# Kernel tuning notes

Measured on AMD Instinct MI355X. Metric: run time of the kernel, lower is better.

## Reference

```python
import jax, jax.numpy as jnp
import numpy as np

E, H, F, LE, LD, K, CD, DIN = 256, 8, 1024, 4, 3, 8, 4, 4
B, S = 16, 512
SIG2 = 1.0 ** 2 + 1e-8   # dr_sigma**2 + 1e-8
EPS = 1e-5               # LayerNorm / BatchNorm eps


def _ln(x, w, b):
    m = x.mean(-1, keepdims=True)
    v = ((x - m) ** 2).mean(-1, keepdims=True)
    return (x - m) / jnp.sqrt(v + EPS) * w + b


def _gelu(x):
    return jax.nn.gelu(x, approximate=False)  # torch nn.GELU default = exact erf


def _mha(xq, xkv, qkv_w, qkv_b, out_w, out_b, bias=None):
    # torch nn.MultiheadAttention (batch_first), additive float attn bias broadcast over heads
    wq, wk, wv = jnp.split(qkv_w, 3, axis=0)
    bq, bk, bv = jnp.split(qkv_b, 3)
    q = xq @ wq.T + bq
    k = xkv @ wk.T + bk
    v = xkv @ wv.T + bv
    Bn, Tq, Tk = q.shape[0], q.shape[1], k.shape[1]
    hd = E // H
    qh = q.reshape(Bn, Tq, H, hd)
    kh = k.reshape(Bn, Tk, H, hd)
    vh = v.reshape(Bn, Tk, H, hd)
    s = jnp.einsum('bqhd,bkhd->bhqk', qh, kh) / jnp.sqrt(jnp.asarray(hd, q.dtype))
    if bias is not None:
        s = s + bias[:, None]  # same bias for every head
    p = jax.nn.softmax(s, axis=-1)
    o = jnp.einsum('bhqk,bkhd->bqhd', p, vh).reshape(Bn, Tq, E)
    return o @ out_w.T + out_b


def _forward(x, mask, parent_idx, in_w, in_b, bn_w, bn_b, dr_gamma,
             e_qkv_w, e_qkv_b, e_out_w, e_out_b, e_l1_w, e_l1_b, e_l2_w, e_l2_b,
             e_n1_w, e_n1_b, e_n2_w, e_n2_b,
             parent_w, parent_b, query_embed, c1_w, c1_b, c2_w, c2_b,
             d_sqkv_w, d_sqkv_b, d_sout_w, d_sout_b,
             d_cqkv_w, d_cqkv_b, d_cout_w, d_cout_b,
             d_l1_w, d_l1_b, d_l2_w, d_l2_b,
             d_n1_w, d_n1_b, d_n2_w, d_n2_b, d_n3_w, d_n3_b,
             child_w, child_b, o1_w, o1_b, o2_w, o2_b):
    x = jnp.nan_to_num(x)
    # input_dim==4 convention: (log_pt, dEta, dPhi, log_E)
    coords = jnp.stack([x[..., 1], x[..., 2]], axis=-1)          # [B,S,2]
    # input_proj: Linear -> BatchNorm1d (eval: mean 0, var 1) -> GELU (dropout=identity in eval)
    h = x @ in_w.T + in_b
    h = (h / jnp.sqrt(1.0 + EPS)) * bn_w + bn_b
    h = _gelu(h)
    # dR Gaussian attention bias: [B,S,S]; mask is all-valid so no -inf fill
    d = coords[:, :, None, :] - coords[:, None, :, :]
    dr2 = d[..., 0] ** 2 + d[..., 1] ** 2
    bias = -(dr_gamma[0] * dr2) / (2.0 * SIG2)
    # dR-biased pre-norm encoder
    for i in range(LE):
        hn = _ln(h, e_n1_w[i], e_n1_b[i])
        h = h + _mha(hn, hn, e_qkv_w[i], e_qkv_b[i], e_out_w[i], e_out_b[i], bias)
        hn = _ln(h, e_n2_w[i], e_n2_b[i])
        h = h + _gelu(hn @ e_l1_w[i].T + e_l1_b[i]) @ e_l2_w[i].T + e_l2_b[i]
    memory = jnp.nan_to_num(h)
    parent_logit = (memory @ parent_w.T + parent_b)[..., 0]       # [B,S]
    # conditional decoder queries
    p = memory[jnp.arange(memory.shape[0]), parent_idx]           # [B,E]
    m = mask.astype(memory.dtype)
    g = (memory * m[..., None]).sum(1) / jnp.maximum(m.sum(1, keepdims=True), 1.0)
    cond = _gelu(jnp.concatenate([p, g], -1) @ c1_w.T + c1_b) @ c2_w.T + c2_b
    t = query_embed[None] + cond[:, None]                         # [B,K,E]
    # pre-norm transformer decoder (self-attn, cross-attn, ff)
    for i in range(LD):
        tn = _ln(t, d_n1_w[i], d_n1_b[i])
        t = t + _mha(tn, tn, d_sqkv_w[i], d_sqkv_b[i], d_sout_w[i], d_sout_b[i])
        tn = _ln(t, d_n2_w[i], d_n2_b[i])
        t = t + _mha(tn, memory, d_cqkv_w[i], d_cqkv_b[i], d_cout_w[i], d_cout_b[i])
        tn = _ln(t, d_n3_w[i], d_n3_b[i])
        t = t + _gelu(tn @ d_l1_w[i].T + d_l1_b[i]) @ d_l2_w[i].T + d_l2_b[i]
    child_feat = t @ child_w.T + child_b                          # [B,K,CD]
    obj_logit = (_gelu(t @ o1_w.T + o1_b) @ o2_w.T + o2_b)[..., 0]  # [B,K]
    return parent_logit, child_feat, obj_logit


def setup_inputs() -> dict:
    key = jax.random.key(0)
    ks = iter(jax.random.split(key, 64))
    def w(shape, scale=0.05):
        return jax.random.normal(next(ks), shape, jnp.float32) * scale
    return {
        'x': jax.random.normal(next(ks), (B, S, DIN), jnp.float32),
        'mask': jnp.ones((B, S), dtype=bool),
        'parent_idx': jax.random.randint(next(ks), (B,), 0, S),
        'in_w': w((E, DIN)), 'in_b': jnp.zeros((E,)),
        'bn_w': jnp.ones((E,)), 'bn_b': jnp.zeros((E,)),
        'dr_gamma': jnp.ones((1,)),
        'e_qkv_w': w((LE, 3 * E, E)), 'e_qkv_b': jnp.zeros((LE, 3 * E)),
        'e_out_w': w((LE, E, E)), 'e_out_b': jnp.zeros((LE, E)),
        'e_l1_w': w((LE, F, E)), 'e_l1_b': jnp.zeros((LE, F)),
        'e_l2_w': w((LE, E, F)), 'e_l2_b': jnp.zeros((LE, E)),
        'e_n1_w': jnp.ones((LE, E)), 'e_n1_b': jnp.zeros((LE, E)),
        'e_n2_w': jnp.ones((LE, E)), 'e_n2_b': jnp.zeros((LE, E)),
        'parent_w': w((1, E)), 'parent_b': jnp.zeros((1,)),
        'query_embed': w((K, E), 0.02),
        'c1_w': w((E, 2 * E)), 'c1_b': jnp.zeros((E,)),
        'c2_w': w((E, E)), 'c2_b': jnp.zeros((E,)),
        'd_sqkv_w': w((LD, 3 * E, E)), 'd_sqkv_b': jnp.zeros((LD, 3 * E)),
        'd_sout_w': w((LD, E, E)), 'd_sout_b': jnp.zeros((LD, E)),
        'd_cqkv_w': w((LD, 3 * E, E)), 'd_cqkv_b': jnp.zeros((LD, 3 * E)),
        'd_cout_w': w((LD, E, E)), 'd_cout_b': jnp.zeros((LD, E)),
        'd_l1_w': w((LD, F, E)), 'd_l1_b': jnp.zeros((LD, F)),
        'd_l2_w': w((LD, E, F)), 'd_l2_b': jnp.zeros((LD, E)),
        'd_n1_w': jnp.ones((LD, E)), 'd_n1_b': jnp.zeros((LD, E)),
        'd_n2_w': jnp.ones((LD, E)), 'd_n2_b': jnp.zeros((LD, E)),
        'd_n3_w': jnp.ones((LD, E)), 'd_n3_b': jnp.zeros((LD, E)),
        'child_w': w((CD, E)), 'child_b': jnp.zeros((CD,)),
        'o1_w': w((E, E)), 'o1_b': jnp.zeros((E,)),
        'o2_w': w((1, E)), 'o2_b': jnp.zeros((1,)),
    }


def reference(x, mask, parent_idx, in_w, in_b, bn_w, bn_b, dr_gamma,
              e_qkv_w, e_qkv_b, e_out_w, e_out_b, e_l1_w, e_l1_b, e_l2_w, e_l2_b,
              e_n1_w, e_n1_b, e_n2_w, e_n2_b,
              parent_w, parent_b, query_embed, c1_w, c1_b, c2_w, c2_b,
              d_sqkv_w, d_sqkv_b, d_sout_w, d_sout_b,
              d_cqkv_w, d_cqkv_b, d_cout_w, d_cout_b,
              d_l1_w, d_l1_b, d_l2_w, d_l2_b,
              d_n1_w, d_n1_b, d_n2_w, d_n2_b, d_n3_w, d_n3_b,
              child_w, child_b, o1_w, o1_b, o2_w, o2_b):
    return _forward(x, mask, parent_idx, in_w, in_b, bn_w, bn_b, dr_gamma,
                    e_qkv_w, e_qkv_b, e_out_w, e_out_b, e_l1_w, e_l1_b, e_l2_w, e_l2_b,
                    e_n1_w, e_n1_b, e_n2_w, e_n2_b,
                    parent_w, parent_b, query_embed, c1_w, c1_b, c2_w, c2_b,
                    d_sqkv_w, d_sqkv_b, d_sout_w, d_sout_b,
                    d_cqkv_w, d_cqkv_b, d_cout_w, d_cout_b,
                    d_l1_w, d_l1_b, d_l2_w, d_l2_b,
                    d_n1_w, d_n1_b, d_n2_w, d_n2_b, d_n3_w, d_n3_b,
                    child_w, child_b, o1_w, o1_b, o2_w, o2_b)
```

## Files before the change

kernel.cpp:

```cpp
#include <hip/hip_runtime.h>
#include <math.h>

#define E 256
#define H 8
#define HD 32
#define FF 1024
#define LE 4
#define LDN 3
#define KQ 8
#define CDIM 4
#define DIN 4
#define BATCH 16
#define SEQ 512

typedef __attribute__((ext_vector_type(8))) short s8b;
typedef __attribute__((ext_vector_type(4))) float f32x4;

__device__ __forceinline__ float gelu_f(float x) {
  return 0.5f * x * (1.f + erff(x * 0.70710678118654752f));
}

__device__ __forceinline__ unsigned short f2b(float f) {
  union { float f; unsigned u; } a;
  a.f = f;
  unsigned r = (a.u + 0x7fffu + ((a.u >> 16) & 1u)) >> 16;
  return (unsigned short)r;
}

__device__ __forceinline__ float b2f(unsigned short u) {
  union { unsigned u; float f; } a;
  a.u = ((unsigned)u) << 16;
  return a.f;
}

__device__ __forceinline__ void gload16(const unsigned short* g, unsigned short* l) {
  __builtin_amdgcn_global_load_lds((const __attribute__((address_space(1))) void*)g,
                                   (__attribute__((address_space(3))) void*)l, 16, 0, 0);
}

template <int GELU, int RESID, int OMODE>
__global__ __launch_bounds__(256) void mfma_gemm_kernel(
    const unsigned short* __restrict__ A, const unsigned short* __restrict__ Wt,
    const float* __restrict__ bias, const float* __restrict__ resid,
    float* __restrict__ outf, unsigned short* __restrict__ outb,
    unsigned short* __restrict__ vtb,
    int M, int N, int K) {
  __shared__ __align__(16) unsigned short As[128 * 32];
  __shared__ __align__(16) unsigned short Bs[128 * 32];
  int tid = threadIdx.x;
  int lane = tid & 63, w = tid >> 6;
  int row0 = blockIdx.y * 128, col0 = blockIdx.x * 128;
  int wr = (w >> 1) * 64, wc = (w & 1) * 64;
  f32x4 acc[4][4] = {};

  int sr0 = w * 32 + (lane >> 2);
  int sr1 = sr0 + 16;
  int sc = lane & 3;
  int gc0 = (sc ^ ((sr0 >> 1) & 3)) * 8;
  int gc1 = (sc ^ ((sr1 >> 1) & 3)) * 8;
  const unsigned short* Ap0 = A + (size_t)(row0 + sr0) * K + gc0;
  const unsigned short* Ap1 = A + (size_t)(row0 + sr1) * K + gc1;
  const unsigned short* Bp0 = Wt + (size_t)(col0 + sr0) * K + gc0;
  const unsigned short* Bp1 = Wt + (size_t)(col0 + sr1) * K + gc1;
  unsigned short* lA0 = As + (w * 32) * 32;
  unsigned short* lA1 = As + (w * 32 + 16) * 32;
  unsigned short* lB0 = Bs + (w * 32) * 32;
  unsigned short* lB1 = Bs + (w * 32 + 16) * 32;

  for (int k0 = 0; k0 < K; k0 += 32) {
    __syncthreads();
    gload16(Ap0 + k0, lA0);
    gload16(Ap1 + k0, lA1);
    gload16(Bp0 + k0, lB0);
    gload16(Bp1 + k0, lB1);
    __syncthreads();
    int krow = lane & 15, kq = lane >> 4;
    s8b afr[4], bfr[4];
    #pragma unroll
    for (int mi = 0; mi < 4; ++mi) {
      int r = wr + mi * 16 + krow;
      afr[mi] = *(const s8b*)(As + r * 32 + ((kq ^ ((r >> 1) & 3)) * 8));
    }
    #pragma unroll
    for (int ni = 0; ni < 4; ++ni) {
      int r = wc + ni * 16 + krow;
      bfr[ni] = *(const s8b*)(Bs + r * 32 + ((kq ^ ((r >> 1) & 3)) * 8));
    }
    #pragma unroll
    for (int mi = 0; mi < 4; ++mi)
      #pragma unroll
      for (int ni = 0; ni < 4; ++ni)
        acc[mi][ni] = __builtin_amdgcn_mfma_f32_16x16x32_bf16(afr[mi], bfr[ni], acc[mi][ni], 0, 0, 0);
  }

  int cl = lane & 15, rb = (lane >> 4) * 4;
  #pragma unroll
  for (int ni = 0; ni < 4; ++ni) {
    int col = col0 + wc + ni * 16 + cl;
    float bv = bias[col];
    #pragma unroll
    for (int mi = 0; mi < 4; ++mi) {
      #pragma unroll
      for (int j = 0; j < 4; ++j) {
        int row = row0 + wr + mi * 16 + rb + j;
        float v = acc[mi][ni][j] + bv;
        if (RESID) v += resid[(size_t)row * N + col];
        if (GELU) v = gelu_f(v);
        if (OMODE == 0) {
          outf[(size_t)row * N + col] = v;
        } else if (OMODE == 1) {
          outb[(size_t)row * N + col] = f2b(v);
        } else {
          int b = row >> 9, s = row & 511;
          int sect = col >> 8, hh = (col >> 5) & 7, d = col & 31;
          if (sect < 2)
            outb[((((size_t)sect * BATCH + b) * H + hh) * SEQ + s) * HD + d] = f2b(v);
          else
            vtb[(((size_t)b * H + hh) * HD + d) * SEQ + s] = f2b(v);
        }
      }
    }
  }
}

__global__ __launch_bounds__(256) void mfma_gemm64_kernel(
    const unsigned short* __restrict__ A, const unsigned short* __restrict__ Wt,
    const float* __restrict__ bias, const float* __restrict__ resid,
    float* __restrict__ outf, int M, int N, int K) {
  __shared__ __align__(16) unsigned short As[64 * 32];
  __shared__ __align__(16) unsigned short Bs[128 * 32];
  int tid = threadIdx.x;
  int lane = tid & 63, w = tid >> 6;
  int row0 = blockIdx.y * 64, col0 = blockIdx.x * 128;
  int wr = (w >> 1) * 32, wc = (w & 1) * 64;
  f32x4 acc[2][4] = {};

  int sc = lane & 3;
  int srA = w * 16 + (lane >> 2);
  int gcA = (sc ^ ((srA >> 1) & 3)) * 8;
  const unsigned short* ApA = A + (size_t)(row0 + srA) * K + gcA;
  unsigned short* lA = As + (w * 16) * 32;
  int sr0 = w * 32 + (lane >> 2);
  int sr1 = sr0 + 16;
  int gc0 = (sc ^ ((sr0 >> 1) & 3)) * 8;
  int gc1 = (sc ^ ((sr1 >> 1) & 3)) * 8;
  const unsigned short* Bp0 = Wt + (size_t)(col0 + sr0) * K + gc0;
  const unsigned short* Bp1 = Wt + (size_t)(col0 + sr1) * K + gc1;
  unsigned short* lB0 = Bs + (w * 32) * 32;
  unsigned short* lB1 = Bs + (w * 32 + 16) * 32;

  for (int k0 = 0; k0 < K; k0 += 32) {
    __syncthreads();
    gload16(ApA + k0, lA);
    gload16(Bp0 + k0, lB0);
    gload16(Bp1 + k0, lB1);
    __syncthreads();
    int krow = lane & 15, kq = lane >> 4;
    s8b afr[2], bfr[4];
    #pragma unroll
    for (int mi = 0; mi < 2; ++mi) {
      int r = wr + mi * 16 + krow;
      afr[mi] = *(const s8b*)(As + r * 32 + ((kq ^ ((r >> 1) & 3)) * 8));
    }
    #pragma unroll
    for (int ni = 0; ni < 4; ++ni) {
      int r = wc + ni * 16 + krow;
      bfr[ni] = *(const s8b*)(Bs + r * 32 + ((kq ^ ((r >> 1) & 3)) * 8));
    }
    #pragma unroll
    for (int mi = 0; mi < 2; ++mi)
      #pragma unroll
      for (int ni = 0; ni < 4; ++ni)
        acc[mi][ni] = __builtin_amdgcn_mfma_f32_16x16x32_bf16(afr[mi], bfr[ni], acc[mi][ni], 0, 0, 0);
  }

  int cl = lane & 15, rb = (lane >> 4) * 4;
  #pragma unroll
  for (int ni = 0; ni < 4; ++ni) {
    int col = col0 + wc + ni * 16 + cl;
    float bv = bias[col];
    #pragma unroll
    for (int mi = 0; mi < 2; ++mi) {
      #pragma unroll
      for (int j = 0; j < 4; ++j) {
        int row = row0 + wr + mi * 16 + rb + j;
        float v = acc[mi][ni][j] + bv + resid[(size_t)row * N + col];
        outf[(size_t)row * N + col] = v;
      }
    }
  }
}

__global__ __launch_bounds__(256) void mfma_attn_kernel(
    const unsigned short* __restrict__ qkb, const unsigned short* __restrict__ vt,
    const float2* __restrict__ carr, const float* __restrict__ gamma_p,
    unsigned short* __restrict__ out) {
  __shared__ __align__(16) unsigned short P[4][16 * 64];
  int tid = threadIdx.x, lane = tid & 63, w = tid >> 6;
  int qt = blockIdx.x, h = blockIdx.y, b = blockIdx.z;
  int q0 = qt * 64 + w * 16;
  const unsigned short* qh = qkb + (((size_t)b * H + h) * SEQ) * HD;
  const unsigned short* kh = qkb + ((((size_t)BATCH + b) * H + h) * SEQ) * HD;
  const unsigned short* vh = vt + (((size_t)b * H + h) * HD) * SEQ;
  int r16 = lane & 15, q4 = lane >> 4;
  s8b qa = *(const s8b*)(qh + (size_t)(q0 + r16) * HD + q4 * 8);
  float eq[4], pq[4];
  #pragma unroll
  for (int j = 0; j < 4; ++j) {
    float2 c = carr[b * SEQ + q0 + q4 * 4 + j];
    eq[j] = c.x; pq[j] = c.y;
  }
  float gam = gamma_p[0] * 0.49999999500000004f;
  const float scale = 0.17677669529663687f;
  float m[4], lsum[4];
  #pragma unroll
  for (int j = 0; j < 4; ++j) { m[j] = -1e30f; lsum[j] = 0.f; }
  f32x4 o0 = {}, o1 = {};
  const f32x4 zf = {0.f, 0.f, 0.f, 0.f};
  unsigned short* pw = &P[w][0];

  for (int t = 0; t < SEQ / 64; ++t) {
    int k0 = t * 64;
    f32x4 sf[4];
    #pragma unroll
    for (int f = 0; f < 4; ++f) {
      s8b bk = *(const s8b*)(kh + (size_t)(k0 + f * 16 + r16) * HD + q4 * 8);
      sf[f] = __builtin_amdgcn_mfma_f32_16x16x32_bf16(qa, bk, zf, 0, 0, 0);
    }
    float ek[4], pk[4];
    #pragma unroll
    for (int f = 0; f < 4; ++f) {
      float2 c = carr[b * SEQ + k0 + f * 16 + r16];
      ek[f] = c.x; pk[f] = c.y;
    }
    float sc_[4][4];
    float tmax[4] = {-1e30f, -1e30f, -1e30f, -1e30f};
    #pragma unroll
    for (int f = 0; f < 4; ++f)
      #pragma unroll
      for (int j = 0; j < 4; ++j) {
        float de = eq[j] - ek[f], dp = pq[j] - pk[f];
        float v = sf[f][j] * scale - gam * (de * de + dp * dp);
        sc_[f][j] = v;
        tmax[j] = fmaxf(tmax[j], v);
      }
    #pragma unroll
    for (int j = 0; j < 4; ++j) {
      #pragma unroll
      for (int off = 1; off < 16; off <<= 1)
        tmax[j] = fmaxf(tmax[j], __shfl_xor(tmax[j], off));
      float mn = fmaxf(m[j], tmax[j]);
      float al = __expf(m[j] - mn);
      m[j] = mn;
      lsum[j] *= al;
      o0[j] *= al;
      o1[j] *= al;
    }
    __syncthreads();
    #pragma unroll
    for (int f = 0; f < 4; ++f)
      #pragma unroll
      for (int j = 0; j < 4; ++j) {
        float p = __expf(sc_[f][j] - m[j]);
        lsum[j] += p;
        int prow = q4 * 4 + j;
        int c = f * 16 + r16;
        int chunk = (c >> 3) ^ (prow & 7);
        pw[prow * 64 + chunk * 8 + (c & 7)] = f2b(p);
      }
    __syncthreads();
    #pragma unroll
    for (int ks = 0; ks < 2; ++ks) {
      int chunk = (ks * 4 + q4) ^ (r16 & 7);
      s8b pa = *(const s8b*)(pw + r16 * 64 + chunk * 8);
      s8b v0 = *(const s8b*)(vh + (size_t)r16 * SEQ + k0 + ks * 32 + q4 * 8);
      s8b v1 = *(const s8b*)(vh + (size_t)(16 + r16) * SEQ + k0 + ks * 32 + q4 * 8);
      o0 = __builtin_amdgcn_mfma_f32_16x16x32_bf16(pa, v0, o0, 0, 0, 0);
      o1 = __builtin_amdgcn_mfma_f32_16x16x32_bf16(pa, v1, o1, 0, 0, 0);
    }
  }
  #pragma unroll
  for (int j = 0; j < 4; ++j) {
    #pragma unroll
    for (int off = 1; off < 16; off <<= 1)
      lsum[j] += __shfl_xor(lsum[j], off);
    float inv = 1.f / lsum[j];
    size_t rbase = ((size_t)(b * SEQ + q0 + q4 * 4 + j)) * E + h * HD;
    out[rbase + r16] = f2b(o0[j] * inv);
    out[rbase + 16 + r16] = f2b(o1[j] * inv);
  }
}

__global__ void coords_kernel(const float* __restrict__ x, float2* __restrict__ carr) {
  int i = blockIdx.x * 256 + threadIdx.x;
  if (i >= BATCH * SEQ) return;
  carr[i] = make_float2(x[(size_t)i * DIN + 1], x[(size_t)i * DIN + 2]);
}

__global__ void f2b_kernel(const float* __restrict__ in, unsigned short* __restrict__ out, int n4) {
  int i = blockIdx.x * 256 + threadIdx.x;
  if (i >= n4) return;
  float4 v = ((const float4*)in)[i];
  ushort4 o;
  o.x = f2b(v.x); o.y = f2b(v.y); o.z = f2b(v.z); o.w = f2b(v.w);
  ((ushort4*)out)[i] = o;
}

__global__ void kvw_remap_kernel(const float* __restrict__ w, const float* __restrict__ b,
                                 unsigned short* __restrict__ wout, float* __restrict__ bout) {
  int i = blockIdx.x * 256 + threadIdx.x;
  if (i < 1536) bout[i] = b[(i >> 9) * 768 + 256 + (i & 511)];
  if (i >= 98304) return;
  int row = i >> 6, cc = i & 63;
  int l = row >> 9, rr = row & 511;
  const float* src = w + ((size_t)l * 768 + 256 + rr) * 256 + cc * 4;
  float4 v = *(const float4*)src;
  ushort4 o;
  o.x = f2b(v.x); o.y = f2b(v.y); o.z = f2b(v.z); o.w = f2b(v.w);
  *(ushort4*)(wout + (size_t)row * 256 + cc * 4) = o;
}


template <int N, int GELU>
__global__ __launch_bounds__(256) void dec_ln_gemv_kernel(
    const float* __restrict__ t, const float* __restrict__ nw, const float* __restrict__ nb,
    const float* __restrict__ W, const float* __restrict__ bias, float* __restrict__ outg) {
  __shared__ float X[8][256];
  __shared__ float Pp[4][64][9];
  int b = blockIdx.x, by = blockIdx.y, tid = threadIdx.x;
  const float* tg = t + (size_t)b * 2048;
  int w = tid >> 6, l = tid & 63;
  #pragma unroll
  for (int rr = 0; rr < 2; ++rr) {
    int r = w * 2 + rr;
    float v0 = tg[r * 256 + l], v1 = tg[r * 256 + 64 + l];
    float v2 = tg[r * 256 + 128 + l], v3 = tg[r * 256 + 192 + l];
    float s = v0 + v1 + v2 + v3;
    for (int o = 32; o > 0; o >>= 1) s += __shfl_xor(s, o);
    float mean = s * (1.f / 256);
    float d0 = v0 - mean, d1 = v1 - mean, d2 = v2 - mean, d3 = v3 - mean;
    float var = d0 * d0 + d1 * d1 + d2 * d2 + d3 * d3;
    for (int o = 32; o > 0; o >>= 1) var += __shfl_xor(var, o);
    float inv = rsqrtf(var * (1.f / 256) + 1e-5f);
    X[r][l] = d0 * inv * nw[l] + nb[l];
    X[r][l + 64] = d1 * inv * nw[l + 64] + nb[l + 64];
    X[r][l + 128] = d2 * inv * nw[l + 128] + nb[l + 128];
    X[r][l + 192] = d3 * inv * nw[l + 192] + nb[l + 192];
  }
  __syncthreads();
  int j = tid & 63, kq = tid >> 6;
  int col = by * 64 + j;
  const float4* wp = (const float4*)(W + (size_t)col * 256 + kq * 64);
  float acc[8] = {};
  #pragma unroll
  for (int kk = 0; kk < 16; ++kk) {
    float4 wv = wp[kk];
    int base = kq * 64 + kk * 4;
    #pragma unroll
    for (int r = 0; r < 8; ++r) {
      float4 xv = *(const float4*)&X[r][base];
      acc[r] += xv.x * wv.x + xv.y * wv.y + xv.z * wv.z + xv.w * wv.w;
    }
  }
  #pragma unroll
  for (int r = 0; r < 8; ++r) Pp[kq][j][r] = acc[r];
  __syncthreads();
  for (int i = tid; i < 512; i += 256) {
    int r = i & 7, j2 = i >> 3;
    float v = Pp[0][j2][r] + Pp[1][j2][r] + Pp[2][j2][r] + Pp[3][j2][r] + bias[by * 64 + j2];
    if (GELU) v = gelu_f(v);
    outg[((size_t)b * 8 + r) * N + by * 64 + j2] = v;
  }
}

__global__ __launch_bounds__(256) void dec_selfattn_sout_kernel(
    const float* __restrict__ qkvg, const float* __restrict__ W, const float* __restrict__ bias,
    float* __restrict__ t) {
  __shared__ float QK[8][768];
  __shared__ float S[512];
  __shared__ float X[8][256];
  __shared__ float Pp[4][64][9];
  int b = blockIdx.x, by = blockIdx.y, tid = threadIdx.x;
  const float* qg = qkvg + (size_t)b * 8 * 768;
  for (int i = tid; i < 6144; i += 256) ((float*)QK)[i] = qg[i];
  __syncthreads();
  for (int t2 = tid; t2 < 512; t2 += 256) {
    int h = t2 >> 6, q = (t2 >> 3) & 7, k = t2 & 7;
    const float* qp = &QK[q][h * 32];
    const float* kp = &QK[k][256 + h * 32];
    float d = 0.f;
    #pragma unroll
    for (int jj = 0; jj < 32; ++jj) d += qp[jj] * kp[jj];
    S[t2] = d * 0.17677669529663687f;
  }
  __syncthreads();
  if (tid < 64) {
    float* row = &S[tid * 8];
    float m = row[0];
    #pragma unroll
    for (int k = 1; k < 8; ++k) m = fmaxf(m, row[k]);
    float sum = 0.f;
    #pragma unroll
    for (int k = 0; k < 8; ++k) { float e = __expf(row[k] - m); row[k] = e; sum += e; }
    float inv = 1.f / sum;
    #pragma unroll
    for (int k = 0; k < 8; ++k) row[k] *= inv;
  }
  __syncthreads();
  for (int i = tid; i < 2048; i += 256) {
    int q = i >> 8, c = i & 255, h = c >> 5;
    const float* pr = &S[h * 64 + q * 8];
    float acc = 0.f;
    #pragma unroll
    for (int k = 0; k < 8; ++k) acc += pr[k] * QK[k][512 + c];
    X[q][c] = acc;
  }
  __syncthreads();
  int j = tid & 63, kq = tid >> 6;
  int col = by * 64 + j;
  const float4* wp = (const float4*)(W + (size_t)col * 256 + kq * 64);
  float acc[8] = {};
  #pragma unroll
  for (int kk = 0; kk < 16; ++kk) {
    float4 wv = wp[kk];
    int base = kq * 64 + kk * 4;
    #pragma unroll
    for (int r = 0; r < 8; ++r) {
      float4 xv = *(const float4*)&X[r][base];
      acc[r] += xv.x * wv.x + xv.y * wv.y + xv.z * wv.z + xv.w * wv.w;
    }
  }
  #pragma unroll
  for (int r = 0; r < 8; ++r) Pp[kq][j][r] = acc[r];
  __syncthreads();
  for (int i = tid; i < 512; i += 256) {
    int r = i & 7, j2 = i >> 3;
    float v = Pp[0][j2][r] + Pp[1][j2][r] + Pp[2][j2][r] + Pp[3][j2][r] + bias[by * 64 + j2];
    t[((size_t)b * 8 + r) * 256 + by * 64 + j2] += v;
  }
}

__global__ __launch_bounds__(256) void dec_gemv_resid_kernel(
    const float* __restrict__ Xg, const float* __restrict__ W, const float* __restrict__ bias,
    float* __restrict__ t) {
  __shared__ float X[8][256];
  __shared__ float Pp[4][64][9];
  int b = blockIdx.x, by = blockIdx.y, tid = threadIdx.x;
  const float* xg = Xg + (size_t)b * 2048;
  for (int i = tid; i < 2048; i += 256) ((float*)X)[i] = xg[i];
  __syncthreads();
  int j = tid & 63, kq = tid >> 6;
  int col = by * 64 + j;
  const float4* wp = (const float4*)(W + (size_t)col * 256 + kq * 64);
  float acc[8] = {};
  #pragma unroll
  for (int kk = 0; kk < 16; ++kk) {
    float4 wv = wp[kk];
    int base = kq * 64 + kk * 4;
    #pragma unroll
    for (int r = 0; r < 8; ++r) {
      float4 xv = *(const float4*)&X[r][base];
      acc[r] += xv.x * wv.x + xv.y * wv.y + xv.z * wv.z + xv.w * wv.w;
    }
  }
  #pragma unroll
  for (int r = 0; r < 8; ++r) Pp[kq][j][r] = acc[r];
  __syncthreads();
  for (int i = tid; i < 512; i += 256) {
    int r = i & 7, j2 = i >> 3;
    float v = Pp[0][j2][r] + Pp[1][j2][r] + Pp[2][j2][r] + Pp[3][j2][r] + bias[by * 64 + j2];
    t[((size_t)b * 8 + r) * 256 + by * 64 + j2] += v;
  }
}

__global__ __launch_bounds__(256) void dec_ffn2_kernel(
    const float* __restrict__ MIDg, const float* __restrict__ W, const float* __restrict__ bias,
    float* __restrict__ t) {
  __shared__ float X[8][1024];
  __shared__ float Pp[4][64][9];
  int b = blockIdx.x, by = blockIdx.y, tid = threadIdx.x;
  const float* xg = MIDg + (size_t)b * 8192;
  for (int i = tid; i < 8192; i += 256) ((float*)X)[i] = xg[i];
  __syncthreads();
  int j = tid & 63, kq = tid >> 6;
  int col = by * 64 + j;
  const float4* wp = (const float4*)(W + (size_t)col * 1024 + kq * 256);
  float acc[8] = {};
  #pragma unroll 8
  for (int kk = 0; kk < 64; ++kk) {
    float4 wv = wp[kk];
    int base = kq * 256 + kk * 4;
    #pragma unroll
    for (int r = 0; r < 8; ++r) {
      float4 xv = *(const float4*)&X[r][base];
      acc[r] += xv.x * wv.x + xv.y * wv.y + xv.z * wv.z + xv.w * wv.w;
    }
  }
  #pragma unroll
  for (int r = 0; r < 8; ++r) Pp[kq][j][r] = acc[r];
  __syncthreads();
  for (int i = tid; i < 512; i += 256) {
    int r = i & 7, j2 = i >> 3;
    float v = Pp[0][j2][r] + Pp[1][j2][r] + Pp[2][j2][r] + Pp[3][j2][r] + bias[by * 64 + j2];
    t[((size_t)b * 8 + r) * 256 + by * 64 + j2] += v;
  }
}

__global__ __launch_bounds__(256) void cross_attn_kernel(
    const float* __restrict__ Q, const unsigned short* __restrict__ KV,
    int koff, int voff, float* __restrict__ out) {
  __shared__ float sv[512];
  __shared__ float red[256];
  __shared__ float qv[32];
  __shared__ float pvred[8][32];
  int tid = threadIdx.x;
  int bid = blockIdx.x;
  int q = bid % KQ;
  int h = (bid / KQ) % H;
  int b = bid / (KQ * H);
  if (tid < 32) qv[tid] = Q[((size_t)(b * KQ + q)) * E + h * HD + tid];
  __syncthreads();
  const float scale = 0.17677669529663687f;
  for (int k = tid; k < SEQ; k += 256) {
    const unsigned short* kp = KV + ((size_t)(b * SEQ + k)) * 1536 + koff + h * HD;
    float d = 0.f;
    #pragma unroll
    for (int j4 = 0; j4 < 4; ++j4) {
      s8b kv8 = *(const s8b*)(kp + j4 * 8);
      #pragma unroll
      for (int j = 0; j < 8; ++j)
        d += qv[j4 * 8 + j] * b2f((unsigned short)kv8[j]);
    }
    sv[k] = d * scale;
  }
  __syncthreads();
  float m = -1e30f;
  for (int k = tid; k < SEQ; k += 256) m = fmaxf(m, sv[k]);
  red[tid] = m; __syncthreads();
  for (int s = 128; s > 0; s >>= 1) {
    if (tid < s) red[tid] = fmaxf(red[tid], red[tid + s]);
    __syncthreads();
  }
  m = red[0]; __syncthreads();
  float lsum = 0.f;
  for (int k = tid; k < SEQ; k += 256) { float e = __expf(sv[k] - m); sv[k] = e; lsum += e; }
  red[tid] = lsum; __syncthreads();
  for (int s = 128; s > 0; s >>= 1) {
    if (tid < s) red[tid] += red[tid + s];
    __syncthreads();
  }
  float denom = red[0];
  int d = tid & 31, g = tid >> 5;
  float acc = 0.f;
  for (int k = g; k < SEQ; k += 8)
    acc += sv[k] * b2f(KV[((size_t)(b * SEQ + k)) * 1536 + voff + h * HD + d]);
  pvred[g][d] = acc;
  __syncthreads();
  if (tid < 32) {
    float r = 0.f;
    #pragma unroll
    for (int gg = 0; gg < 8; ++gg) r += pvred[gg][tid];
    out[((size_t)(b * KQ + q)) * E + h * HD + tid] = r / denom;
  }
}

__global__ void ln_bf16_kernel(const float* __restrict__ in, const float* __restrict__ w,
                               const float* __restrict__ b, unsigned short* __restrict__ out) {
  int r = blockIdx.x;
  int l = threadIdx.x;
  const float* p = in + (size_t)r * E;
  float v0 = p[l], v1 = p[l + 64], v2 = p[l + 128], v3 = p[l + 192];
  float s = v0 + v1 + v2 + v3;
  for (int off = 32; off > 0; off >>= 1) s += __shfl_xor(s, off);
  float mean = s * (1.f / E);
  float d0 = v0 - mean, d1 = v1 - mean, d2 = v2 - mean, d3 = v3 - mean;
  float var = d0 * d0 + d1 * d1 + d2 * d2 + d3 * d3;
  for (int off = 32; off > 0; off >>= 1) var += __shfl_xor(var, off);
  float inv = rsqrtf(var * (1.f / E) + 1e-5f);
  unsigned short* o = out + (size_t)r * E;
  o[l]       = f2b(d0 * inv * w[l]       + b[l]);
  o[l + 64]  = f2b(d1 * inv * w[l + 64]  + b[l + 64]);
  o[l + 128] = f2b(d2 * inv * w[l + 128] + b[l + 128]);
  o[l + 192] = f2b(d3 * inv * w[l + 192] + b[l + 192]);
}

__global__ void input_proj_kernel(const float* __restrict__ x, const float* __restrict__ in_w,
                                  const float* __restrict__ in_b, const float* __restrict__ bn_w,
                                  const float* __restrict__ bn_b, float* __restrict__ h) {
  int idx = blockIdx.x * 256 + threadIdx.x;
  int row = idx >> 8, e = idx & 255;
  const float* xr = x + (size_t)row * DIN;
  float v = in_b[e];
  #pragma unroll
  for (int i = 0; i < DIN; ++i) v += xr[i] * in_w[e * DIN + i];
  v = v * (1.0f / sqrtf(1.0f + 1e-5f)) * bn_w[e] + bn_b[e];
  h[idx] = gelu_f(v);
}

__global__ __launch_bounds__(256) void pool_gather_kernel(
    const float* __restrict__ mem, const int* __restrict__ pidx, float* __restrict__ pg) {
  __shared__ float red[8][32];
  int b = blockIdx.x, cy = blockIdx.y, tid = threadIdx.x;
  int c = cy * 32 + (tid & 31), g = tid >> 5;
  float s = 0.f;
  for (int r = g; r < SEQ; r += 8)
    s += mem[((size_t)b * SEQ + r) * E + c];
  red[g][tid & 31] = s;
  __syncthreads();
  if (tid < 32) {
    float t = 0.f;
    #pragma unroll
    for (int g2 = 0; g2 < 8; ++g2) t += red[g2][tid];
    pg[(size_t)b * 512 + 256 + cy * 32 + tid] = t * (1.f / SEQ);
    pg[(size_t)b * 512 + cy * 32 + tid] = mem[((size_t)b * SEQ + pidx[b]) * E + cy * 32 + tid];
  }
}

__global__ void cond_kernel(const float* __restrict__ pg, const float* __restrict__ c1w,
                            const float* __restrict__ c1b, const float* __restrict__ c2w,
                            const float* __restrict__ c2b, const float* __restrict__ qe,
                            float* __restrict__ t) {
  __shared__ float PG[512];
  __shared__ float C1[256];
  int b = blockIdx.x, c = threadIdx.x;
  PG[c] = pg[(size_t)b * 512 + c];
  PG[c + 256] = pg[(size_t)b * 512 + 256 + c];
  __syncthreads();
  const float4* wp = (const float4*)(c1w + (size_t)c * 512);
  float acc = c1b[c];
  #pragma unroll 8
  for (int kk = 0; kk < 128; ++kk) {
    float4 wv = wp[kk];
    int base = kk * 4;
    acc += PG[base] * wv.x + PG[base + 1] * wv.y + PG[base + 2] * wv.z + PG[base + 3] * wv.w;
  }
  C1[c] = gelu_f(acc);
  __syncthreads();
  const float4* wp2 = (const float4*)(c2w + (size_t)c * 256);
  float acc2 = c2b[c];
  #pragma unroll 8
  for (int kk = 0; kk < 64; ++kk) {
    float4 wv = wp2[kk];
    int base = kk * 4;
    acc2 += C1[base] * wv.x + C1[base + 1] * wv.y + C1[base + 2] * wv.z + C1[base + 3] * wv.w;
  }
  #pragma unroll
  for (int k = 0; k < KQ; ++k)
    t[((size_t)b * KQ + k) * E + c] = qe[k * E + c] + acc2;
}

__global__ void head_kernel(const float* __restrict__ t,
                            const float* __restrict__ childw, const float* __restrict__ childb,
                            const float* __restrict__ o1w, const float* __restrict__ o1b,
                            const float* __restrict__ o2w, const float* __restrict__ o2b,
                            float* __restrict__ out_child, float* __restrict__ out_obj) {
  __shared__ float tr[256];
  __shared__ float red[256];
  int r = blockIdx.x, c = threadIdx.x;
  tr[c] = t[(size_t)r * E + c];
  __syncthreads();
  const float4* wp = (const float4*)(o1w + (size_t)c * 256);
  float acc = o1b[c];
  #pragma unroll 8
  for (int kk = 0; kk < 64; ++kk) {
    float4 wv = wp[kk];
    int base = kk * 4;
    acc += tr[base] * wv.x + tr[base + 1] * wv.y + tr[base + 2] * wv.z + tr[base + 3] * wv.w;
  }
  red[c] = gelu_f(acc) * o2w[c];
  __syncthreads();
  for (int s = 128; s > 0; s >>= 1) {
    if (c < s) red[c] += red[c + s];
    __syncthreads();
  }
  if (c == 0) out_obj[r] = red[0] + o2b[0];
  __syncthreads();
  #pragma unroll
  for (int j = 0; j < CDIM; ++j) {
    red[c] = tr[c] * childw[j * E + c];
    __syncthreads();
    for (int s = 128; s > 0; s >>= 1) {
      if (c < s) red[c] += red[c + s];
      __syncthreads();
    }
    if (c == 0) out_child[r * CDIM + j] = red[0] + childb[j];
    __syncthreads();
  }
}

__global__ void rowdot_kernel(const float* __restrict__ A, const float* __restrict__ w,
                              const float* __restrict__ bias, float* __restrict__ out) {
  int r = blockIdx.x, l = threadIdx.x;
  const float* p = A + (size_t)r * E;
  float s = p[l] * w[l] + p[l + 64] * w[l + 64] + p[l + 128] * w[l + 128] + p[l + 192] * w[l + 192];
  for (int off = 32; off > 0; off >>= 1) s += __shfl_xor(s, off);
  if (l == 0) out[r] = s + bias[0];
}

extern "C" void kernel_launch(void* const* d_in, const int* in_sizes, int n_in,
                              void* d_out, int out_size, void* d_ws, size_t ws_size,
                              hipStream_t stream) {
  const float* x          = (const float*)d_in[0];
  const int*   parent_idx = (const int*)d_in[2];
  const float* in_w  = (const float*)d_in[3];
  const float* in_b  = (const float*)d_in[4];
  const float* bn_w  = (const float*)d_in[5];
  const float* bn_b  = (const float*)d_in[6];
  const float* dr_gamma = (const float*)d_in[7];
  const float* e_qkv_w = (const float*)d_in[8];
  const float* e_qkv_b = (const float*)d_in[9];
  const float* e_out_w = (const float*)d_in[10];
  const float* e_out_b = (const float*)d_in[11];
  const float* e_l1_w = (const float*)d_in[12];
  const float* e_l1_b = (const float*)d_in[13];
  const float* e_l2_w = (const float*)d_in[14];
  const float* e_l2_b = (const float*)d_in[15];
  const float* e_n1_w = (const float*)d_in[16];
  const float* e_n1_b = (const float*)d_in[17];
  const float* e_n2_w = (const float*)d_in[18];
  const float* e_n2_b = (const float*)d_in[19];
  const float* parent_w = (const float*)d_in[20];
  const float* parent_b = (const float*)d_in[21];
  const float* query_embed = (const float*)d_in[22];
  const float* c1_w = (const float*)d_in[23];
  const float* c1_b = (const float*)d_in[24];
  const float* c2_w = (const float*)d_in[25];
  const float* c2_b = (const float*)d_in[26];
  const float* d_sqkv_w = (const float*)d_in[27];
  const float* d_sqkv_b = (const float*)d_in[28];
  const float* d_sout_w = (const float*)d_in[29];
  const float* d_sout_b = (const float*)d_in[30];
  const float* d_cqkv_w = (const float*)d_in[31];
  const float* d_cqkv_b = (const float*)d_in[32];
  const float* d_cout_w = (const float*)d_in[33];
  const float* d_cout_b = (const float*)d_in[34];
  const float* d_l1_w = (const float*)d_in[35];
  const float* d_l1_b = (const float*)d_in[36];
  const float* d_l2_w = (const float*)d_in[37];
  const float* d_l2_b = (const float*)d_in[38];
  const float* d_n1_w = (const float*)d_in[39];
  const float* d_n1_b = (const float*)d_in[40];
  const float* d_n2_w = (const float*)d_in[41];
  const float* d_n2_b = (const float*)d_in[42];
  const float* d_n3_w = (const float*)d_in[43];
  const float* d_n3_b = (const float*)d_in[44];
  const float* child_w = (const float*)d_in[45];
  const float* child_b = (const float*)d_in[46];
  const float* o1_w = (const float*)d_in[47];
  const float* o1_b = (const float*)d_in[48];
  const float* o2_w = (const float*)d_in[49];
  const float* o2_b = (const float*)d_in[50];

  float* out = (float*)d_out;
  const int ROWS = BATCH * SEQ;
  const int TROWS = BATCH * KQ;

  float* ws = (float*)d_ws;
  float* h         = ws;
  float* attnout_d = h + (size_t)ROWS * E;
  float* pg        = attnout_d + (size_t)TROWS * E;
  float* tbuf      = pg + BATCH * 2 * E;
  float* q_t       = tbuf + (size_t)TROWS * E;
  float* qkv_t     = q_t + (size_t)TROWS * E;
  float* dmid      = qkv_t + (size_t)TROWS * 3 * E;
  float* kvb3      = dmid + (size_t)TROWS * FF;
  unsigned short* kv_bf   = (unsigned short*)(kvb3 + 1536);
  unsigned short* hn_bf   = kv_bf + (size_t)ROWS * 1536;
  unsigned short* attn_bf = hn_bf + (size_t)ROWS * E;
  unsigned short* mid_bf  = attn_bf + (size_t)ROWS * E;
  unsigned short* eqkv_bf = mid_bf + (size_t)ROWS * FF;
  unsigned short* eout_bf = eqkv_bf + (size_t)LE * 3 * E * E;
  unsigned short* el1_bf  = eout_bf + (size_t)LE * E * E;
  unsigned short* el2_bf  = el1_bf + (size_t)LE * FF * E;
  unsigned short* kvw_bf  = el2_bf + (size_t)LE * E * FF;
  float2* carr = (float2*)(kvw_bf + (size_t)1536 * 256);
  unsigned short* qkb = mid_bf;
  unsigned short* vtb = mid_bf + (size_t)2 * ROWS * E;

  auto cvt = [&](const float* src, unsigned short* dst, size_t n) {
    int n4 = (int)(n / 4);
    f2b_kernel<<<(n4 + 255) / 256, 256, 0, stream>>>(src, dst, n4);
  };

  cvt(e_qkv_w, eqkv_bf, (size_t)LE * 3 * E * E);
  cvt(e_out_w, eout_bf, (size_t)LE * E * E);
  cvt(e_l1_w, el1_bf, (size_t)LE * FF * E);
  cvt(e_l2_w, el2_bf, (size_t)LE * E * FF);
  kvw_remap_kernel<<<384, 256, 0, stream>>>(d_cqkv_w, d_cqkv_b, kvw_bf, kvb3);
  coords_kernel<<<(BATCH * SEQ + 255) / 256, 256, 0, stream>>>(x, carr);

  input_proj_kernel<<<ROWS, 256, 0, stream>>>(x, in_w, in_b, bn_w, bn_b, h);

  for (int i = 0; i < LE; ++i) {
    const float* qb = e_qkv_b + (size_t)i * 3 * E;
    const float* ob = e_out_b + (size_t)i * E;
    const float* l1b = e_l1_b + (size_t)i * FF;
    const float* l2b = e_l2_b + (size_t)i * E;
    ln_bf16_kernel<<<ROWS, 64, 0, stream>>>(h, e_n1_w + i * E, e_n1_b + i * E, hn_bf);
    mfma_gemm_kernel<0, 0, 2><<<dim3(6, 64), 256, 0, stream>>>(
        hn_bf, eqkv_bf + (size_t)i * 3 * E * E, qb, nullptr, nullptr, qkb, vtb, ROWS, 3 * E, E);
    mfma_attn_kernel<<<dim3(SEQ / 64, H, BATCH), 256, 0, stream>>>(qkb, vtb, carr, dr_gamma, attn_bf);
    mfma_gemm64_kernel<<<dim3(2, 128), 256, 0, stream>>>(
        attn_bf, eout_bf + (size_t)i * E * E, ob, h, h, ROWS, E, E);
    ln_bf16_kernel<<<ROWS, 64, 0, stream>>>(h, e_n2_w + i * E, e_n2_b + i * E, hn_bf);
    mfma_gemm_kernel<1, 0, 1><<<dim3(8, 64), 256, 0, stream>>>(
        hn_bf, el1_bf + (size_t)i * FF * E, l1b, nullptr, nullptr, mid_bf, nullptr, ROWS, FF, E);
    mfma_gemm64_kernel<<<dim3(2, 128), 256, 0, stream>>>(
        mid_bf, el2_bf + (size_t)i * E * FF, l2b, h, h, ROWS, E, FF);
  }

  rowdot_kernel<<<ROWS, 64, 0, stream>>>(h, parent_w, parent_b, out);

  pool_gather_kernel<<<dim3(BATCH, 8), 256, 0, stream>>>(h, parent_idx, pg);
  cond_kernel<<<BATCH, 256, 0, stream>>>(pg, c1_w, c1_b, c2_w, c2_b, query_embed, tbuf);

  cvt(h, hn_bf, (size_t)ROWS * E);
  mfma_gemm_kernel<0, 0, 1><<<dim3(12, 64), 256, 0, stream>>>(
      hn_bf, kvw_bf, kvb3, nullptr, nullptr, kv_bf, nullptr, ROWS, 3 * E * 2, E);

  for (int i = 0; i < LDN; ++i) {
    dec_ln_gemv_kernel<768, 0><<<dim3(BATCH, 12), 256, 0, stream>>>(
        tbuf, d_n1_w + i * E, d_n1_b + i * E,
        d_sqkv_w + (size_t)i * 3 * E * E, d_sqkv_b + (size_t)i * 3 * E, qkv_t);
    dec_selfattn_sout_kernel<<<dim3(BATCH, 4), 256, 0, stream>>>(
        qkv_t, d_sout_w + (size_t)i * E * E, d_sout_b + (size_t)i * E, tbuf);
    dec_ln_gemv_kernel<256, 0><<<dim3(BATCH, 4), 256, 0, stream>>>(
        tbuf, d_n2_w + i * E, d_n2_b + i * E,
        d_cqkv_w + (size_t)i * 3 * E * E, d_cqkv_b + (size_t)i * 3 * E, q_t);
    cross_attn_kernel<<<BATCH * H * KQ, 256, 0, stream>>>(
        q_t, kv_bf, i * 512, i * 512 + 256, attnout_d);
    dec_gemv_resid_kernel<<<dim3(BATCH, 4), 256, 0, stream>>>(
        attnout_d, d_cout_w + (size_t)i * E * E, d_cout_b + (size_t)i * E, tbuf);
    dec_ln_gemv_kernel<1024, 1><<<dim3(BATCH, 16), 256, 0, stream>>>(
        tbuf, d_n3_w + i * E, d_n3_b + i * E,
        d_l1_w + (size_t)i * FF * E, d_l1_b + (size_t)i * FF, dmid);
    dec_ffn2_kernel<<<dim3(BATCH, 4), 256, 0, stream>>>(
        dmid, d_l2_w + (size_t)i * E * FF, d_l2_b + (size_t)i * E, tbuf);
  }

  head_kernel<<<TROWS, 256, 0, stream>>>(tbuf, child_w, child_b, o1_w, o1_b, o2_w, o2_b,
                                         out + ROWS, out + ROWS + TROWS * CDIM);
}
```

Before: 804.9 us.

## Fuse LayerNorm into residual GEMM epilogues and retile encoder GEMMs to 64-row blocks

Residual-add GEMMs now compute full 256-wide rows per block, so the epilogue can apply the next LayerNorm and write the bf16 normalized activations directly. This removes the standalone LayerNorm kernels and the final fp32-to-bf16 conversion. The input projection also applies the first LayerNorm. The remaining GEMMs switch from 128x128 to 64x128 tiles, which doubles the grid. The trade-off is that the N=256 fused GEMM launches only 128 blocks with 16 accumulators per wave, which lowers parallelism for those GEMMs.

```diff
diff --git a/kernel.cpp b/kernel.cpp
--- a/kernel.cpp
+++ b/kernel.cpp
@@ -38,95 +38,11 @@
                                    (__attribute__((address_space(3))) void*)l, 16, 0, 0);
 }
 
-template <int GELU, int RESID, int OMODE>
-__global__ __launch_bounds__(256) void mfma_gemm_kernel(
+template <int GELU, int OMODE>
+__global__ __launch_bounds__(256) void mfma_gemm64o_kernel(
     const unsigned short* __restrict__ A, const unsigned short* __restrict__ Wt,
-    const float* __restrict__ bias, const float* __restrict__ resid,
-    float* __restrict__ outf, unsigned short* __restrict__ outb,
-    unsigned short* __restrict__ vtb,
-    int M, int N, int K) {
-  __shared__ __align__(16) unsigned short As[128 * 32];
-  __shared__ __align__(16) unsigned short Bs[128 * 32];
-  int tid = threadIdx.x;
-  int lane = tid & 63, w = tid >> 6;
-  int row0 = blockIdx.y * 128, col0 = blockIdx.x * 128;
-  int wr = (w >> 1) * 64, wc = (w & 1) * 64;
-  f32x4 acc[4][4] = {};
-
-  int sr0 = w * 32 + (lane >> 2);
-  int sr1 = sr0 + 16;
-  int sc = lane & 3;
-  int gc0 = (sc ^ ((sr0 >> 1) & 3)) * 8;
-  int gc1 = (sc ^ ((sr1 >> 1) & 3)) * 8;
-  const unsigned short* Ap0 = A + (size_t)(row0 + sr0) * K + gc0;
-  const unsigned short* Ap1 = A + (size_t)(row0 + sr1) * K + gc1;
-  const unsigned short* Bp0 = Wt + (size_t)(col0 + sr0) * K + gc0;
-  const unsigned short* Bp1 = Wt + (size_t)(col0 + sr1) * K + gc1;
-  unsigned short* lA0 = As + (w * 32) * 32;
-  unsigned short* lA1 = As + (w * 32 + 16) * 32;
-  unsigned short* lB0 = Bs + (w * 32) * 32;
-  unsigned short* lB1 = Bs + (w * 32 + 16) * 32;
-
-  for (int k0 = 0; k0 < K; k0 += 32) {
-    __syncthreads();
-    gload16(Ap0 + k0, lA0);
-    gload16(Ap1 + k0, lA1);
-    gload16(Bp0 + k0, lB0);
-    gload16(Bp1 + k0, lB1);
-    __syncthreads();
-    int krow = lane & 15, kq = lane >> 4;
-    s8b afr[4], bfr[4];
-    #pragma unroll
-    for (int mi = 0; mi < 4; ++mi) {
-      int r = wr + mi * 16 + krow;
-      afr[mi] = *(const s8b*)(As + r * 32 + ((kq ^ ((r >> 1) & 3)) * 8));
-    }
-    #pragma unroll
-    for (int ni = 0; ni < 4; ++ni) {
-      int r = wc + ni * 16 + krow;
-      bfr[ni] = *(const s8b*)(Bs + r * 32 + ((kq ^ ((r >> 1) & 3)) * 8));
-    }
-    #pragma unroll
-    for (int mi = 0; mi < 4; ++mi)
-      #pragma unroll
-      for (int ni = 0; ni < 4; ++ni)
-        acc[mi][ni] = __builtin_amdgcn_mfma_f32_16x16x32_bf16(afr[mi], bfr[ni], acc[mi][ni], 0, 0, 0);
-  }
-
-  int cl = lane & 15, rb = (lane >> 4) * 4;
-  #pragma unroll
-  for (int ni = 0; ni < 4; ++ni) {
-    int col = col0 + wc + ni * 16 + cl;
-    float bv = bias[col];
-    #pragma unroll
-    for (int mi = 0; mi < 4; ++mi) {
-      #pragma unroll
-      for (int j = 0; j < 4; ++j) {
-        int row = row0 + wr + mi * 16 + rb + j;
-        float v = acc[mi][ni][j] + bv;
-        if (RESID) v += resid[(size_t)row * N + col];
-        if (GELU) v = gelu_f(v);
-        if (OMODE == 0) {
-          outf[(size_t)row * N + col] = v;
-        } else if (OMODE == 1) {
-          outb[(size_t)row * N + col] = f2b(v);
-        } else {
-          int b = row >> 9, s = row & 511;
-          int sect = col >> 8, hh = (col >> 5) & 7, d = col & 31;
-          if (sect < 2)
-            outb[((((size_t)sect * BATCH + b) * H + hh) * SEQ + s) * HD + d] = f2b(v);
-          else
-            vtb[(((size_t)b * H + hh) * HD + d) * SEQ + s] = f2b(v);
-        }
-      }
-    }
-  }
-}
-
-__global__ __launch_bounds__(256) void mfma_gemm64_kernel(
-    const unsigned short* __restrict__ A, const unsigned short* __restrict__ Wt,
-    const float* __restrict__ bias, const float* __restrict__ resid,
-    float* __restrict__ outf, int M, int N, int K) {
+    const float* __restrict__ bias, unsigned short* __restrict__ outb,
+    unsigned short* __restrict__ vtb, int N, int K) {
   __shared__ __align__(16) unsigned short As[64 * 32];
   __shared__ __align__(16) unsigned short Bs[128 * 32];
   int tid = threadIdx.x;
@@ -184,8 +100,112 @@
       #pragma unroll
       for (int j = 0; j < 4; ++j) {
         int row = row0 + wr + mi * 16 + rb + j;
-        float v = acc[mi][ni][j] + bv + resid[(size_t)row * N + col];
-        outf[(size_t)row * N + col] = v;
+        float v = acc[mi][ni][j] + bv;
+        if (GELU) v = gelu_f(v);
+        if (OMODE == 1) {
+          outb[(size_t)row * N + col] = f2b(v);
+        } else {
+          int b = row >> 9, s = row & 511;
+          int sect = col >> 8, hh = (col >> 5) & 7, d = col & 31;
+          if (sect < 2)
+            outb[((((size_t)sect * BATCH + b) * H + hh) * SEQ + s) * HD + d] = f2b(v);
+          else
+            vtb[(((size_t)b * H + hh) * HD + d) * SEQ + s] = f2b(v);
+        }
+      }
+    }
+  }
+}
+
+template <int LNMODE>
+__global__ __launch_bounds__(256) void mfma_gemm_n256_ln_kernel(
+    const unsigned short* __restrict__ A, const unsigned short* __restrict__ Wt,
+    const float* __restrict__ bias, float* __restrict__ h,
+    const float* __restrict__ nw, const float* __restrict__ nb,
+    unsigned short* __restrict__ hn, int K) {
+  __shared__ __align__(16) unsigned short As[64 * 32];
+  __shared__ __align__(16) unsigned short Bs[256 * 32];
+  int tid = threadIdx.x;
+  int lane = tid & 63, w = tid >> 6;
+  int row0 = blockIdx.x * 64;
+  f32x4 acc[16] = {};
+
+  int sc = lane & 3;
+  int srA = w * 16 + (lane >> 2);
+  int gcA = (sc ^ ((srA >> 1) & 3)) * 8;
+  const unsigned short* ApA = A + (size_t)(row0 + srA) * K + gcA;
+  unsigned short* lA = As + (w * 16) * 32;
+  int srB[4], gcB[4];
+  const unsigned short* BpB[4];
+  unsigned short* lB[4];
+  #pragma unroll
+  for (int is = 0; is < 4; ++is) {
+    srB[is] = w * 64 + is * 16 + (lane >> 2);
+    gcB[is] = (sc ^ ((srB[is] >> 1) & 3)) * 8;
+    BpB[is] = Wt + (size_t)srB[is] * K + gcB[is];
+    lB[is] = Bs + (w * 64 + is * 16) * 32;
+  }
+
+  for (int k0 = 0; k0 < K; k0 += 32) {
+    __syncthreads();
+    gload16(ApA + k0, lA);
+    #pragma unroll
+    for (int is = 0; is < 4; ++is) gload16(BpB[is] + k0, lB[is]);
+    __syncthreads();
+    int krow = lane & 15, kq = lane >> 4;
+    int ra = w * 16 + krow;
+    s8b afr = *(const s8b*)(As + ra * 32 + ((kq ^ ((ra >> 1) & 3)) * 8));
+    #pragma unroll
+    for (int nf = 0; nf < 16; ++nf) {
+      int r = nf * 16 + krow;
+      s8b bfr = *(const s8b*)(Bs + r * 32 + ((kq ^ ((r >> 1) & 3)) * 8));
+      acc[nf] = __builtin_amdgcn_mfma_f32_16x16x32_bf16(afr, bfr, acc[nf], 0, 0, 0);
+    }
+  }
+
+  int cl = lane & 15, quad = lane >> 4;
+  #pragma unroll
+  for (int nf = 0; nf < 16; ++nf) {
+    int col = nf * 16 + cl;
+    float bv = bias[col];
+    #pragma unroll
+    for (int j = 0; j < 4; ++j) {
+      int row = row0 + w * 16 + quad * 4 + j;
+      float v = acc[nf][j] + bv + h[(size_t)row * 256 + col];
+      acc[nf][j] = v;
+      h[(size_t)row * 256 + col] = v;
+    }
+  }
+  if (LNMODE == 0) {
+    #pragma unroll
+    for (int j = 0; j < 4; ++j) {
+      int row = row0 + w * 16 + quad * 4 + j;
+      float s = 0.f;
+      #pragma unroll
+      for (int nf = 0; nf < 16; ++nf) s += acc[nf][j];
+      s += __shfl_xor(s, 1); s += __shfl_xor(s, 2);
+      s += __shfl_xor(s, 4); s += __shfl_xor(s, 8);
+      float mean = s * (1.f / 256);
+      float var = 0.f;
+      #pragma unroll
+      for (int nf = 0; nf < 16; ++nf) { float d = acc[nf][j] - mean; var += d * d; }
+      var += __shfl_xor(var, 1); var += __shfl_xor(var, 2);
+      var += __shfl_xor(var, 4); var += __shfl_xor(var, 8);
+      float inv = rsqrtf(var * (1.f / 256) + 1e-5f);
+      #pragma unroll
+      for (int nf = 0; nf < 16; ++nf) {
+        int col = nf * 16 + cl;
+        hn[(size_t)row * 256 + col] = f2b((acc[nf][j] - mean) * inv * nw[col] + nb[col]);
+      }
+    }
+  } else {
+    #pragma unroll
+    for (int nf = 0; nf < 16; ++nf) {
+      int col = nf * 16 + cl;
+      #pragma unroll
+      for (int j = 0; j < 4; ++j) {
+        int row = row0 + w * 16 + quad * 4 + j;
+        hn[(size_t)row * 256 + col] = f2b(acc[nf][j]);
       }
     }
   }
@@ -318,6 +338,38 @@
   ushort4 o;
   o.x = f2b(v.x); o.y = f2b(v.y); o.z = f2b(v.z); o.w = f2b(v.w);
   *(ushort4*)(wout + (size_t)row * 256 + cc * 4) = o;
+}
+
+__global__ __launch_bounds__(256) void input_proj_ln_kernel(
+    const float* __restrict__ x, const float* __restrict__ in_w, const float* __restrict__ in_b,
+    const float* __restrict__ bn_w, const float* __restrict__ bn_b,
+    const float* __restrict__ nw, const float* __restrict__ nb,
+    float* __restrict__ h, unsigned short* __restrict__ hn) {
+  __shared__ float sred[4];
+  __shared__ float vred[4];
+  int row = blockIdx.x, e = threadIdx.x;
+  const float* xr = x + (size_t)row * DIN;
+  float v = in_b[e];
+  #pragma unroll
+  for (int i = 0; i < DIN; ++i) v += xr[i] * in_w[e * DIN + i];
+  v = v * (1.0f / sqrtf(1.0f + 1e-5f)) * bn_w[e] + bn_b[e];
+  v = gelu_f(v);
+  h[(size_t)row * 256 + e] = v;
+  int lane = e & 63, w = e >> 6;
+  float s = v;
+  #pragma unroll
+  for (int off = 32; off > 0; off >>= 1) s += __shfl_xor(s, off);
+  if (lane == 0) sred[w] = s;
+  __syncthreads();
+  float mean = (sred[0] + sred[1] + sred[2] + sred[3]) * (1.f / 256);
+  float d = v - mean;
+  float vr = d * d;
+  #pragma unroll
+  for (int off = 32; off > 0; off >>= 1) vr += __shfl_xor(vr, off);
+  if (lane == 0) vred[w] = vr;
+  __syncthreads();
+  float inv = rsqrtf((vred[0] + vred[1] + vred[2] + vred[3]) * (1.f / 256) + 1e-5f);
+  hn[(size_t)row * 256 + e] = f2b(d * inv * nw[e] + nb[e]);
 }
 
 
@@ -562,39 +614,6 @@
     for (int gg = 0; gg < 8; ++gg) r += pvred[gg][tid];
     out[((size_t)(b * KQ + q)) * E + h * HD + tid] = r / denom;
   }
-}
-
-__global__ void ln_bf16_kernel(const float* __restrict__ in, const float* __restrict__ w,
-                               const float* __restrict__ b, unsigned short* __restrict__ out) {
-  int r = blockIdx.x;
-  int l = threadIdx.x;
-  const float* p = in + (size_t)r * E;
-  float v0 = p[l], v1 = p[l + 64], v2 = p[l + 128], v3 = p[l + 192];
-  float s = v0 + v1 + v2 + v3;
-  for (int off = 32; off > 0; off >>= 1) s += __shfl_xor(s, off);
-  float mean = s * (1.f / E);
-  float d0 = v0 - mean, d1 = v1 - mean, d2 = v2 - mean, d3 = v3 - mean;
-  float var = d0 * d0 + d1 * d1 + d2 * d2 + d3 * d3;
-  for (int off = 32; off > 0; off >>= 1) var += __shfl_xor(var, off);
-  float inv = rsqrtf(var * (1.f / E) + 1e-5f);
-  unsigned short* o = out + (size_t)r * E;
-  o[l]       = f2b(d0 * inv * w[l]       + b[l]);
-  o[l + 64]  = f2b(d1 * inv * w[l + 64]  + b[l + 64]);
-  o[l + 128] = f2b(d2 * inv * w[l + 128] + b[l + 128]);
-  o[l + 192] = f2b(d3 * inv * w[l + 192] + b[l + 192]);
-}
-
-__global__ void input_proj_kernel(const float* __restrict__ x, const float* __restrict__ in_w,
-                                  const float* __restrict__ in_b, const float* __restrict__ bn_w,
-                                  const float* __restrict__ bn_b, float* __restrict__ h) {
-  int idx = blockIdx.x * 256 + threadIdx.x;
-  int row = idx >> 8, e = idx & 255;
-  const float* xr = x + (size_t)row * DIN;
-  float v = in_b[e];
-  #pragma unroll
-  for (int i = 0; i < DIN; ++i) v += xr[i] * in_w[e * DIN + i];
-  v = v * (1.0f / sqrtf(1.0f + 1e-5f)) * bn_w[e] + bn_b[e];
-  h[idx] = gelu_f(v);
 }
 
 __global__ __launch_bounds__(256) void pool_gather_kernel(
@@ -789,24 +808,30 @@
   kvw_remap_kernel<<<384, 256, 0, stream>>>(d_cqkv_w, d_cqkv_b, kvw_bf, kvb3);
   coords_kernel<<<(BATCH * SEQ + 255) / 256, 256, 0, stream>>>(x, carr);
 
-  input_proj_kernel<<<ROWS, 256, 0, stream>>>(x, in_w, in_b, bn_w, bn_b, h);
+  input_proj_ln_kernel<<<ROWS, 256, 0, stream>>>(x, in_w, in_b, bn_w, bn_b,
+                                                 e_n1_w, e_n1_b, h, hn_bf);
 
   for (int i = 0; i < LE; ++i) {
     const float* qb = e_qkv_b + (size_t)i * 3 * E;
     const float* ob = e_out_b + (size_t)i * E;
     const float* l1b = e_l1_b + (size_t)i * FF;
     const float* l2b = e_l2_b + (size_t)i * E;
-    ln_bf16_kernel<<<ROWS, 64, 0, stream>>>(h, e_n1_w + i * E, e_n1_b + i * E, hn_bf);
-    mfma_gemm_kernel<0, 0, 2><<<dim3(6, 64), 256, 0, stream>>>(
-        hn_bf, eqkv_bf + (size_t)i * 3 * E * E, qb, nullptr, nullptr, qkb, vtb, ROWS, 3 * E, E);
+    mfma_gemm64o_kernel<0, 2><<<dim3(6, 128), 256, 0, stream>>>(
+        hn_bf, eqkv_bf + (size_t)i * 3 * E * E, qb, qkb, vtb, 3 * E, E);
     mfma_attn_kernel<<<dim3(SEQ / 64, H, BATCH), 256, 0, stream>>>(qkb, vtb, carr, dr_gamma, attn_bf);
-    mfma_gemm64_kernel<<<dim3(2, 128), 256, 0, stream>>>(
-        attn_bf, eout_bf + (size_t)i * E * E, ob, h, h, ROWS, E, E);
-    ln_bf16_kernel<<<ROWS, 64, 0, stream>>>(h, e_n2_w + i * E, e_n2_b + i * E, hn_bf);
-    mfma_gemm_kernel<1, 0, 1><<<dim3(8, 64), 256, 0, stream>>>(
-        hn_bf, el1_bf + (size_t)i * FF * E, l1b, nullptr, nullptr, mid_bf, nullptr, ROWS, FF, E);
-    mfma_gemm64_kernel<<<dim3(2, 128), 256, 0, stream>>>(
-        mid_bf, el2_bf + (size_t)i * E * FF, l2b, h, h, ROWS, E, FF);
+    mfma_gemm_n256_ln_kernel<0><<<128, 256, 0, stream>>>(
+        attn_bf, eout_bf + (size_t)i * E * E, ob, h,
+        e_n2_w + i * E, e_n2_b + i * E, hn_bf, E);
+    mfma_gemm64o_kernel<1, 1><<<dim3(8, 128), 256, 0, stream>>>(
+        hn_bf, el1_bf + (size_t)i * FF * E, l1b, mid_bf, nullptr, FF, E);
+    if (i < LE - 1)
+      mfma_gemm_n256_ln_kernel<0><<<128, 256, 0, stream>>>(
+          mid_bf, el2_bf + (size_t)i * E * FF, l2b, h,
+          e_n1_w + (i + 1) * E, e_n1_b + (i + 1) * E, hn_bf, FF);
+    else
+      mfma_gemm_n256_ln_kernel<1><<<128, 256, 0, stream>>>(
+          mid_bf, el2_bf + (size_t)i * E * FF, l2b, h,
+          nullptr, nullptr, hn_bf, FF);
   }
 
   rowdot_kernel<<<ROWS, 64, 0, stream>>>(h, parent_w, parent_b, out);
@@ -814,9 +839,8 @@
   pool_gather_kernel<<<dim3(BATCH, 8), 256, 0, stream>>>(h, parent_idx, pg);
   cond_kernel<<<BATCH, 256, 0, stream>>>(pg, c1_w, c1_b, c2_w, c2_b, query_embed, tbuf);
 
-  cvt(h, hn_bf, (size_t)ROWS * E);
-  mfma_gemm_kernel<0, 0, 1><<<dim3(12, 64), 256, 0, stream>>>(
-      hn_bf, kvw_bf, kvb3, nullptr, nullptr, kv_bf, nullptr, ROWS, 3 * E * 2, E);
+  mfma_gemm64o_kernel<0, 1><<<dim3(12, 128), 256, 0, stream>>>(
+      hn_bf, kvw_bf, kvb3, kv_bf, nullptr, 3 * E * 2, E);
 
   for (int i = 0; i < LDN; ++i) {
     dec_ln_gemv_kernel<768, 0><<<dim3(BATCH, 12), 256, 0, stream>>>(
```

New measurement: 814.7 us. Within noise of the previous version (+1.2%).
